# Kernel tuning notes

Hardware: AMD Instinct MI355X
Metric: run time of the kernel (lower is better)

The kernel has to match this reference:

```python
import jax, jax.numpy as jnp
import numpy as np

B, N, E = 4, 2048, 512
H = 8
HD = E // H  # 64
SCALE = HD ** -0.5


def setup_inputs() -> dict:
    key = jax.random.key(0)
    k1, k2, k3 = jax.random.split(key, 3)
    x = jax.random.normal(k1, (B, N, E), dtype=jnp.float32)
    # xavier-uniform-like scaling for weights
    w_qkv = jax.random.normal(k2, (3 * E, E), dtype=jnp.float32) * (2.0 / (4 * E)) ** 0.5
    b_qkv = jnp.zeros((3 * E,), dtype=jnp.float32)
    w_out = jax.random.normal(k3, (E, E), dtype=jnp.float32) * (1.0 / E) ** 0.5
    b_out = jnp.zeros((E,), dtype=jnp.float32)
    return {"x": x, "w_qkv": w_qkv, "b_qkv": b_qkv, "w_out": w_out, "b_out": b_out}


def reference(x, w_qkv, b_qkv, w_out, b_out):
    b_sz, n_patches, _ = x.shape
    # qkv projection: [B,N,3E] -> [B,N,3,H,HD] -> [B,H,3,N,HD]
    qkv = (jnp.einsum('bne,fe->bnf', x, w_qkv) + b_qkv)
    qkv = qkv.reshape(b_sz, n_patches, 3, H, HD).transpose(0, 3, 2, 1, 4)
    q, k, v = qkv[:, :, 0], qkv[:, :, 1], qkv[:, :, 2]  # each [B,H,N,HD]
    attn = jnp.einsum('bhqd,bhkd->bhqk', q * SCALE, k)  # [B,H,N,N]
    attn = jax.nn.softmax(attn, axis=-1)
    # attn_dropout p=0.0 -> identity in reference
    out = jnp.einsum('bhqk,bhkd->bhqd', attn, v)  # [B,H,N,HD]
    out = out.transpose(0, 2, 1, 3).reshape(b_sz, n_patches, E)
    out = jnp.einsum('bne,fe->bnf', out, w_out) + b_out
    return out
```

## Files before the change

kernel.cpp:

```cpp
#include <hip/hip_runtime.h>

#define BB   4
#define SEQ  2048
#define EMB  512
#define NH   8
#define HD   64

typedef __bf16 bf16x8 __attribute__((ext_vector_type(8)));
typedef float  f32x4  __attribute__((ext_vector_type(4)));

__device__ __forceinline__ short f2bf(float f) {
  union { float f; unsigned u; } v; v.f = f;
  unsigned r = v.u + 0x7fffu + ((v.u >> 16) & 1u);
  return (short)(r >> 16);
}

__device__ __forceinline__ void gl_lds16(const void* g, void* l) {
  __builtin_amdgcn_global_load_lds(
      (const __attribute__((address_space(1))) unsigned int*)g,
      (__attribute__((address_space(3))) unsigned int*)l, 16, 0, 0);
}

__global__ __launch_bounds__(256) void cast_f32_bf16(const float* __restrict__ in,
                                                     short* __restrict__ out, int n4) {
  int i = blockIdx.x * 256 + threadIdx.x;
  if (i < n4) {
    float4 v = ((const float4*)in)[i];
    short4 o;
    o.x = f2bf(v.x); o.y = f2bf(v.y); o.z = f2bf(v.z); o.w = f2bf(v.w);
    ((short4*)out)[i] = o;
  }
}

__global__ __launch_bounds__(256) void qkv_gemm(const short* __restrict__ A,
                                                const short* __restrict__ W,
                                                const float* __restrict__ bias,
                                                short* __restrict__ qo,
                                                short* __restrict__ ko,
                                                short* __restrict__ vto) {
  __shared__ __align__(16) short As[128 * 32];
  __shared__ __align__(16) short Bs[128 * 32];
  const int tid  = threadIdx.x;
  const int lane = tid & 63, wave = tid >> 6;
  const int wm = wave >> 1, wf = wave & 1;
  const int col = lane & 15, quad = lane >> 4;
  const int m0 = blockIdx.x * 128, f0 = blockIdx.y * 128;

  f32x4 acc[4][4];
#pragma unroll
  for (int i = 0; i < 4; ++i)
#pragma unroll
    for (int j = 0; j < 4; ++j)
#pragma unroll
      for (int r = 0; r < 4; ++r) acc[i][j][r] = 0.f;

  for (int kt = 0; kt < 512; kt += 32) {
    __syncthreads();
#pragma unroll
    for (int rd = 0; rd < 2; ++rd) {
      int slot = rd * 256 + tid;
      int r = slot >> 2, c8 = (slot & 3) * 8;
      gl_lds16(A + (size_t)(m0 + r) * 512 + kt + c8, (char*)As + rd * 4096 + wave * 1024);
      gl_lds16(W + (size_t)(f0 + r) * 512 + kt + c8, (char*)Bs + rd * 4096 + wave * 1024);
    }
    __syncthreads();
    bf16x8 af[4], bw[4];
#pragma unroll
    for (int i = 0; i < 4; ++i)
      af[i] = *(const bf16x8*)&As[(wm * 64 + i * 16 + col) * 32 + quad * 8];
#pragma unroll
    for (int j = 0; j < 4; ++j)
      bw[j] = *(const bf16x8*)&Bs[(wf * 64 + j * 16 + col) * 32 + quad * 8];
#pragma unroll
    for (int i = 0; i < 4; ++i)
#pragma unroll
      for (int j = 0; j < 4; ++j)
        acc[i][j] = __builtin_amdgcn_mfma_f32_16x16x32_bf16(af[i], bw[j], acc[i][j], 0, 0, 0);
  }

#pragma unroll
  for (int j = 0; j < 4; ++j) {
    const int f = f0 + wf * 64 + j * 16 + col;
    const float bv = bias[f];
    const int sIdx = f >> 9;
    const int h = (f >> 6) & 7;
    const int d = f & 63;
#pragma unroll
    for (int i = 0; i < 4; ++i) {
      const int mbase = m0 + wm * 64 + i * 16 + quad * 4;
      const int b = mbase >> 11;
      const int n = mbase & 2047;
      const size_t bh = (size_t)(b * NH + h);
      if (sIdx == 2) {
        short4 pk;
        pk.x = f2bf(acc[i][j][0] + bv);
        pk.y = f2bf(acc[i][j][1] + bv);
        pk.z = f2bf(acc[i][j][2] + bv);
        pk.w = f2bf(acc[i][j][3] + bv);
        *(short4*)&vto[(bh * HD + d) * SEQ + n] = pk;
      } else {
        short* __restrict__ dst = (sIdx == 0) ? qo : ko;
#pragma unroll
        for (int r = 0; r < 4; ++r)
          dst[(bh * SEQ + n + r) * HD + d] = f2bf(acc[i][j][r] + bv);
      }
    }
  }
}

__global__ __launch_bounds__(256) void attn_kernel(const short* __restrict__ q,
                                                   const short* __restrict__ k,
                                                   const short* __restrict__ vt,
                                                   short* __restrict__ o) {
  __shared__ __align__(16) short Ks[64 * 64];
  __shared__ __align__(16) short Vs[64 * 64];
  __shared__ __align__(16) short Ps[4 * 32 * 72];
  __shared__ float Ls[4 * 32];
  const int tid  = threadIdx.x;
  const int lane = tid & 63, wave = tid >> 6;
  const int col = lane & 15, quad = lane >> 4;
  const int bh = blockIdx.x & 31;
  const int q0 = (blockIdx.x >> 5) * 128;
  const size_t bhBase = (size_t)bh * SEQ * HD;

  bf16x8 qf[2][2];
#pragma unroll
  for (int t = 0; t < 2; ++t)
#pragma unroll
    for (int ks = 0; ks < 2; ++ks)
      qf[t][ks] = *(const bf16x8*)&q[bhBase +
          (size_t)(q0 + wave * 32 + t * 16 + col) * HD + ks * 32 + quad * 8];

  f32x4 oacc[2][4];
#pragma unroll
  for (int t = 0; t < 2; ++t)
#pragma unroll
    for (int nt = 0; nt < 4; ++nt)
#pragma unroll
      for (int r = 0; r < 4; ++r) oacc[t][nt][r] = 0.f;
  float lpart[2] = {0.f, 0.f};

  const int wbase = wave * 32 * 72;

  for (int n0 = 0; n0 < SEQ; n0 += 64) {
    __syncthreads();
#pragma unroll
    for (int c = 0; c < 4; ++c) {
      int slot = (c & 1) * 256 + wave * 64 + lane;
      int row = slot >> 3;
      int cb = (slot & 7) ^ (row & 7);
      if (c < 2)
        gl_lds16(k + bhBase + (size_t)(n0 + row) * HD + cb * 8,
                 (char*)Ks + (c & 1) * 4096 + wave * 1024);
      else
        gl_lds16(vt + bhBase + (size_t)row * SEQ + n0 + cb * 8,
                 (char*)Vs + (c & 1) * 4096 + wave * 1024);
    }
    __syncthreads();

    f32x4 sacc[4][2];
#pragma unroll
    for (int kt = 0; kt < 4; ++kt)
#pragma unroll
      for (int t = 0; t < 2; ++t)
#pragma unroll
        for (int r = 0; r < 4; ++r) sacc[kt][t][r] = 0.f;
#pragma unroll
    for (int kt = 0; kt < 4; ++kt)
#pragma unroll
      for (int ks = 0; ks < 2; ++ks) {
        bf16x8 kf = *(const bf16x8*)&Ks[(kt * 16 + col) * 64 +
                                        (((ks * 4 + quad) ^ (col & 7)) * 8)];
#pragma unroll
        for (int t = 0; t < 2; ++t)
          sacc[kt][t] = __builtin_amdgcn_mfma_f32_16x16x32_bf16(kf, qf[t][ks], sacc[kt][t], 0, 0, 0);
      }

#pragma unroll
    for (int kt = 0; kt < 4; ++kt)
#pragma unroll
      for (int t = 0; t < 2; ++t) {
        float p0 = __expf(0.125f * sacc[kt][t][0]);
        float p1 = __expf(0.125f * sacc[kt][t][1]);
        float p2 = __expf(0.125f * sacc[kt][t][2]);
        float p3 = __expf(0.125f * sacc[kt][t][3]);
        lpart[t] += (p0 + p1) + (p2 + p3);
        short4 pk; pk.x = f2bf(p0); pk.y = f2bf(p1); pk.z = f2bf(p2); pk.w = f2bf(p3);
        *(short4*)&Ps[wbase + (t * 16 + col) * 72 + kt * 16 + quad * 4] = pk;
      }

#pragma unroll
    for (int ks2 = 0; ks2 < 2; ++ks2) {
      bf16x8 pf[2];
#pragma unroll
      for (int t = 0; t < 2; ++t)
        pf[t] = *(const bf16x8*)&Ps[wbase + (t * 16 + col) * 72 + ks2 * 32 + quad * 8];
#pragma unroll
      for (int nt = 0; nt < 4; ++nt) {
        bf16x8 vf = *(const bf16x8*)&Vs[(nt * 16 + col) * 64 +
                                        (((ks2 * 4 + quad) ^ (col & 7)) * 8)];
#pragma unroll
        for (int t = 0; t < 2; ++t)
          oacc[t][nt] = __builtin_amdgcn_mfma_f32_16x16x32_bf16(pf[t], vf, oacc[t][nt], 0, 0, 0);
      }
    }
  }

#pragma unroll
  for (int t = 0; t < 2; ++t) {
    lpart[t] += __shfl_xor(lpart[t], 16);
    lpart[t] += __shfl_xor(lpart[t], 32);
    Ls[wave * 32 + t * 16 + col] = lpart[t];
  }

  const int b = bh >> 3, h = bh & 7;
#pragma unroll
  for (int t = 0; t < 2; ++t) {
    float rl[4];
#pragma unroll
    for (int r = 0; r < 4; ++r)
      rl[r] = 1.0f / Ls[wave * 32 + t * 16 + quad * 4 + r];
#pragma unroll
    for (int nt = 0; nt < 4; ++nt)
#pragma unroll
      for (int r = 0; r < 4; ++r) {
        const int n = q0 + wave * 32 + t * 16 + quad * 4 + r;
        o[((size_t)(b * SEQ + n)) * EMB + h * HD + nt * 16 + col] = f2bf(oacc[t][nt][r] * rl[r]);
      }
  }
}

__global__ __launch_bounds__(256) void proj_gemm(const short* __restrict__ A,
                                                 const short* __restrict__ W,
                                                 const float* __restrict__ bias,
                                                 float* __restrict__ out) {
  __shared__ __align__(16) short As[64 * 32];
  __shared__ __align__(16) short Bs[128 * 32];
  const int tid  = threadIdx.x;
  const int lane = tid & 63, wave = tid >> 6;
  const int wm = wave >> 1, wf = wave & 1;
  const int col = lane & 15, quad = lane >> 4;
  const int m0 = blockIdx.x * 64, f0 = blockIdx.y * 128;

  f32x4 acc[2][4];
#pragma unroll
  for (int i = 0; i < 2; ++i)
#pragma unroll
    for (int j = 0; j < 4; ++j)
#pragma unroll
      for (int r = 0; r < 4; ++r) acc[i][j][r] = 0.f;

  for (int kt = 0; kt < 512; kt += 32) {
    __syncthreads();
    gl_lds16(A + (size_t)(m0 + (tid >> 2)) * 512 + kt + (tid & 3) * 8,
             (char*)As + wave * 1024);
#pragma unroll
    for (int rd = 0; rd < 2; ++rd) {
      int slot = rd * 256 + tid;
      int r = slot >> 2, c8 = (slot & 3) * 8;
      gl_lds16(W + (size_t)(f0 + r) * 512 + kt + c8, (char*)Bs + rd * 4096 + wave * 1024);
    }
    __syncthreads();
    bf16x8 af[2], bw[4];
#pragma unroll
    for (int i = 0; i < 2; ++i)
      af[i] = *(const bf16x8*)&As[(wm * 32 + i * 16 + col) * 32 + quad * 8];
#pragma unroll
    for (int j = 0; j < 4; ++j)
      bw[j] = *(const bf16x8*)&Bs[(wf * 64 + j * 16 + col) * 32 + quad * 8];
#pragma unroll
    for (int i = 0; i < 2; ++i)
#pragma unroll
      for (int j = 0; j < 4; ++j)
        acc[i][j] = __builtin_amdgcn_mfma_f32_16x16x32_bf16(af[i], bw[j], acc[i][j], 0, 0, 0);
  }

#pragma unroll
  for (int j = 0; j < 4; ++j) {
    const int f = f0 + wf * 64 + j * 16 + col;
    const float bv = bias[f];
#pragma unroll
    for (int i = 0; i < 2; ++i) {
      const int mbase = m0 + wm * 32 + i * 16 + quad * 4;
#pragma unroll
      for (int r = 0; r < 4; ++r)
        out[(size_t)(mbase + r) * 512 + f] = acc[i][j][r] + bv;
    }
  }
}

extern "C" void kernel_launch(void* const* d_in, const int* in_sizes, int n_in,
                              void* d_out, int out_size, void* d_ws, size_t ws_size,
                              hipStream_t stream) {
  (void)in_sizes; (void)n_in; (void)out_size; (void)ws_size;
  const float* x     = (const float*)d_in[0];
  const float* w_qkv = (const float*)d_in[1];
  const float* b_qkv = (const float*)d_in[2];
  const float* w_out = (const float*)d_in[3];
  const float* b_out = (const float*)d_in[4];
  float* out = (float*)d_out;

  char* ws = (char*)d_ws;
  short* xb    = (short*)(ws + 0);
  short* wqkvb = (short*)(ws + 8388608);
  short* woutb = (short*)(ws + 9961472);
  short* qb    = (short*)(ws + 10485760);
  short* kb    = (short*)(ws + 18874368);
  short* vtb   = (short*)(ws + 27262976);
  short* ob    = (short*)(ws + 35651584);

  cast_f32_bf16<<<4096, 256, 0, stream>>>(x, xb, 1048576);
  cast_f32_bf16<<<768, 256, 0, stream>>>(w_qkv, wqkvb, 196608);
  cast_f32_bf16<<<256, 256, 0, stream>>>(w_out, woutb, 65536);
  qkv_gemm<<<dim3(64, 12), 256, 0, stream>>>(xb, wqkvb, b_qkv, qb, kb, vtb);
  attn_kernel<<<512, 256, 0, stream>>>(qb, kb, vtb, ob);
  proj_gemm<<<dim3(128, 4), 256, 0, stream>>>(ob, woutb, b_out, out);
}
```

Before: 180.1 us.

## Fuse cast kernels, widen GEMM K-tiles, fold softmax scale into Q with exp2

The three fp32-to-bf16 cast launches become one kernel that uses packed bf16 conversion. Both GEMMs move from a K tile of 32 to 64 with a swizzled LDS layout, halving the number of barrier pairs per K loop. The attention scale times log2(e) is folded into Q at the QKV epilogue, so softmax can use hardware exp2 with no per-element multiply. Attention load and LDS offsets are also precomputed outside the loop. Together these add LDS usage and register pressure, and Q is now stored pre-scaled in bf16, which changes rounding slightly.

After: 169.9 us. 1.06x faster.

```diff
diff --git a/kernel.cpp b/kernel.cpp
--- a/kernel.cpp
+++ b/kernel.cpp
@@ -5,6 +5,7 @@
 #define EMB  512
 #define NH   8
 #define HD   64
+#define QSCALE 0.18033688011f
 
 typedef __bf16 bf16x8 __attribute__((ext_vector_type(8)));
 typedef float  f32x4  __attribute__((ext_vector_type(4)));
@@ -15,21 +16,45 @@
   return (short)(r >> 16);
 }
 
+__device__ __forceinline__ unsigned pk_bf16(float a, float b) {
+#if __has_builtin(__builtin_amdgcn_cvt_pk_bf16_f32)
+  typedef __bf16 bf16v2 __attribute__((ext_vector_type(2)));
+  union { bf16v2 v; unsigned u; } cv;
+  cv.v = __builtin_amdgcn_cvt_pk_bf16_f32(a, b);
+  return cv.u;
+#else
+  return (unsigned)(unsigned short)f2bf(a) | ((unsigned)(unsigned short)f2bf(b) << 16);
+#endif
+}
+
+__device__ __forceinline__ float fexp2(float x) {
+#if __has_builtin(__builtin_amdgcn_exp2f)
+  return __builtin_amdgcn_exp2f(x);
+#else
+  return exp2f(x);
+#endif
+}
+
 __device__ __forceinline__ void gl_lds16(const void* g, void* l) {
   __builtin_amdgcn_global_load_lds(
       (const __attribute__((address_space(1))) unsigned int*)g,
       (__attribute__((address_space(3))) unsigned int*)l, 16, 0, 0);
 }
 
-__global__ __launch_bounds__(256) void cast_f32_bf16(const float* __restrict__ in,
-                                                     short* __restrict__ out, int n4) {
+__global__ __launch_bounds__(256) void cast_all(const float* __restrict__ x,
+                                                const float* __restrict__ wq,
+                                                const float* __restrict__ wo,
+                                                short* __restrict__ xb,
+                                                short* __restrict__ wqb,
+                                                short* __restrict__ wob) {
   int i = blockIdx.x * 256 + threadIdx.x;
-  if (i < n4) {
-    float4 v = ((const float4*)in)[i];
-    short4 o;
-    o.x = f2bf(v.x); o.y = f2bf(v.y); o.z = f2bf(v.z); o.w = f2bf(v.w);
-    ((short4*)out)[i] = o;
-  }
+  const float* src; short* dst; int off;
+  if (i < 1048576)      { src = x;  dst = xb;  off = i; }
+  else if (i < 1245184) { src = wq; dst = wqb; off = i - 1048576; }
+  else                  { src = wo; dst = wob; off = i - 1245184; }
+  float4 v = ((const float4*)src)[off];
+  uint2 o; o.x = pk_bf16(v.x, v.y); o.y = pk_bf16(v.z, v.w);
+  *(uint2*)&dst[off * 4] = o;
 }
 
 __global__ __launch_bounds__(256) void qkv_gemm(const short* __restrict__ A,
@@ -38,14 +63,32 @@
                                                 short* __restrict__ qo,
                                                 short* __restrict__ ko,
                                                 short* __restrict__ vto) {
-  __shared__ __align__(16) short As[128 * 32];
-  __shared__ __align__(16) short Bs[128 * 32];
+  __shared__ __align__(16) short As[128 * 64];
+  __shared__ __align__(16) short Bs[128 * 64];
   const int tid  = threadIdx.x;
   const int lane = tid & 63, wave = tid >> 6;
   const int wm = wave >> 1, wf = wave & 1;
   const int col = lane & 15, quad = lane >> 4;
   const int m0 = blockIdx.x * 128, f0 = blockIdx.y * 128;
 
+  const short* aSrc[4]; const short* wSrc[4];
+#pragma unroll
+  for (int rd = 0; rd < 4; ++rd) {
+    int slot = rd * 256 + tid;
+    int row = slot >> 3;
+    int cb  = (slot & 7) ^ (row & 7);
+    aSrc[rd] = A + (size_t)(m0 + row) * 512 + cb * 8;
+    wSrc[rd] = W + (size_t)(f0 + row) * 512 + cb * 8;
+  }
+  int aOff[2][4], bOff[2][4];
+#pragma unroll
+  for (int kk = 0; kk < 2; ++kk)
+#pragma unroll
+    for (int i = 0; i < 4; ++i) {
+      aOff[kk][i] = (wm * 64 + i * 16 + col) * 64 + (((kk * 4 + quad) ^ (col & 7)) * 8);
+      bOff[kk][i] = (wf * 64 + i * 16 + col) * 64 + (((kk * 4 + quad) ^ (col & 7)) * 8);
+    }
+
   f32x4 acc[4][4];
 #pragma unroll
   for (int i = 0; i < 4; ++i)
@@ -54,28 +97,28 @@
 #pragma unroll
       for (int r = 0; r < 4; ++r) acc[i][j][r] = 0.f;
 
-  for (int kt = 0; kt < 512; kt += 32) {
-    __syncthreads();
-#pragma unroll
-    for (int rd = 0; rd < 2; ++rd) {
-      int slot = rd * 256 + tid;
-      int r = slot >> 2, c8 = (slot & 3) * 8;
-      gl_lds16(A + (size_t)(m0 + r) * 512 + kt + c8, (char*)As + rd * 4096 + wave * 1024);
-      gl_lds16(W + (size_t)(f0 + r) * 512 + kt + c8, (char*)Bs + rd * 4096 + wave * 1024);
-    }
-    __syncthreads();
-    bf16x8 af[4], bw[4];
-#pragma unroll
-    for (int i = 0; i < 4; ++i)
-      af[i] = *(const bf16x8*)&As[(wm * 64 + i * 16 + col) * 32 + quad * 8];
-#pragma unroll
-    for (int j = 0; j < 4; ++j)
-      bw[j] = *(const bf16x8*)&Bs[(wf * 64 + j * 16 + col) * 32 + quad * 8];
-#pragma unroll
-    for (int i = 0; i < 4; ++i)
-#pragma unroll
-      for (int j = 0; j < 4; ++j)
-        acc[i][j] = __builtin_amdgcn_mfma_f32_16x16x32_bf16(af[i], bw[j], acc[i][j], 0, 0, 0);
+  for (int kt = 0; kt < 8; ++kt) {
+    __syncthreads();
+#pragma unroll
+    for (int rd = 0; rd < 4; ++rd) {
+      gl_lds16(aSrc[rd], (char*)As + rd * 4096 + wave * 1024);
+      gl_lds16(wSrc[rd], (char*)Bs + rd * 4096 + wave * 1024);
+      aSrc[rd] += 64; wSrc[rd] += 64;
+    }
+    __syncthreads();
+#pragma unroll
+    for (int kk = 0; kk < 2; ++kk) {
+      bf16x8 af[4], bw[4];
+#pragma unroll
+      for (int i = 0; i < 4; ++i) af[i] = *(const bf16x8*)&As[aOff[kk][i]];
+#pragma unroll
+      for (int j = 0; j < 4; ++j) bw[j] = *(const bf16x8*)&Bs[bOff[kk][j]];
+#pragma unroll
+      for (int i = 0; i < 4; ++i)
+#pragma unroll
+        for (int j = 0; j < 4; ++j)
+          acc[i][j] = __builtin_amdgcn_mfma_f32_16x16x32_bf16(af[i], bw[j], acc[i][j], 0, 0, 0);
+    }
   }
 
 #pragma unroll
@@ -92,17 +135,18 @@
       const int n = mbase & 2047;
       const size_t bh = (size_t)(b * NH + h);
       if (sIdx == 2) {
-        short4 pk;
-        pk.x = f2bf(acc[i][j][0] + bv);
-        pk.y = f2bf(acc[i][j][1] + bv);
-        pk.z = f2bf(acc[i][j][2] + bv);
-        pk.w = f2bf(acc[i][j][3] + bv);
-        *(short4*)&vto[(bh * HD + d) * SEQ + n] = pk;
+        uint2 pk;
+        pk.x = pk_bf16(acc[i][j][0] + bv, acc[i][j][1] + bv);
+        pk.y = pk_bf16(acc[i][j][2] + bv, acc[i][j][3] + bv);
+        *(uint2*)&vto[(bh * HD + d) * SEQ + n] = pk;
+      } else if (sIdx == 0) {
+#pragma unroll
+        for (int r = 0; r < 4; ++r)
+          qo[(bh * SEQ + n + r) * HD + d] = f2bf((acc[i][j][r] + bv) * QSCALE);
       } else {
-        short* __restrict__ dst = (sIdx == 0) ? qo : ko;
 #pragma unroll
         for (int r = 0; r < 4; ++r)
-          dst[(bh * SEQ + n + r) * HD + d] = f2bf(acc[i][j][r] + bv);
+          ko[(bh * SEQ + n + r) * HD + d] = f2bf(acc[i][j][r] + bv);
       }
     }
   }
@@ -131,6 +175,40 @@
       qf[t][ks] = *(const bf16x8*)&q[bhBase +
           (size_t)(q0 + wave * 32 + t * 16 + col) * HD + ks * 32 + quad * 8];
 
+  const int rowL = tid >> 3,         cbL = (tid & 7) ^ (rowL & 7);
+  const int rowH = (256 + tid) >> 3, cbH = (tid & 7) ^ (rowH & 7);
+  const short* ksrcL = k  + bhBase + (size_t)rowL * HD + cbL * 8;
+  const short* ksrcH = k  + bhBase + (size_t)rowH * HD + cbH * 8;
+  const short* vsrcL = vt + bhBase + (size_t)rowL * SEQ + cbL * 8;
+  const short* vsrcH = vt + bhBase + (size_t)rowH * SEQ + cbH * 8;
+  char* ldsKL = (char*)Ks + wave * 1024;
+  char* ldsKH = (char*)Ks + 4096 + wave * 1024;
+  char* ldsVL = (char*)Vs + wave * 1024;
+  char* ldsVH = (char*)Vs + 4096 + wave * 1024;
+
+  const int wbase = wave * 32 * 72;
+  int kfO[4][2], vfO[2][4], pwO[4][2], prO[2][2];
+#pragma unroll
+  for (int kt = 0; kt < 4; ++kt)
+#pragma unroll
+    for (int ks = 0; ks < 2; ++ks)
+      kfO[kt][ks] = (kt * 16 + col) * 64 + (((ks * 4 + quad) ^ (col & 7)) * 8);
+#pragma unroll
+  for (int ks2 = 0; ks2 < 2; ++ks2)
+#pragma unroll
+    for (int nt = 0; nt < 4; ++nt)
+      vfO[ks2][nt] = (nt * 16 + col) * 64 + (((ks2 * 4 + quad) ^ (col & 7)) * 8);
+#pragma unroll
+  for (int kt = 0; kt < 4; ++kt)
+#pragma unroll
+    for (int t = 0; t < 2; ++t)
+      pwO[kt][t] = wbase + (t * 16 + col) * 72 + kt * 16 + quad * 4;
+#pragma unroll
+  for (int t = 0; t < 2; ++t)
+#pragma unroll
+    for (int ks2 = 0; ks2 < 2; ++ks2)
+      prO[t][ks2] = wbase + (t * 16 + col) * 72 + ks2 * 32 + quad * 8;
+
   f32x4 oacc[2][4];
 #pragma unroll
   for (int t = 0; t < 2; ++t)
@@ -140,22 +218,13 @@
       for (int r = 0; r < 4; ++r) oacc[t][nt][r] = 0.f;
   float lpart[2] = {0.f, 0.f};
 
-  const int wbase = wave * 32 * 72;
-
   for (int n0 = 0; n0 < SEQ; n0 += 64) {
     __syncthreads();
-#pragma unroll
-    for (int c = 0; c < 4; ++c) {
-      int slot = (c & 1) * 256 + wave * 64 + lane;
-      int row = slot >> 3;
-      int cb = (slot & 7) ^ (row & 7);
-      if (c < 2)
-        gl_lds16(k + bhBase + (size_t)(n0 + row) * HD + cb * 8,
-                 (char*)Ks + (c & 1) * 4096 + wave * 1024);
-      else
-        gl_lds16(vt + bhBase + (size_t)row * SEQ + n0 + cb * 8,
-                 (char*)Vs + (c & 1) * 4096 + wave * 1024);
-    }
+    gl_lds16(ksrcL, ldsKL);
+    gl_lds16(ksrcH, ldsKH);
+    gl_lds16(vsrcL, ldsVL);
+    gl_lds16(vsrcH, ldsVH);
+    ksrcL += 64 * HD; ksrcH += 64 * HD; vsrcL += 64; vsrcH += 64;
     __syncthreads();
 
     f32x4 sacc[4][2];
@@ -169,8 +238,7 @@
     for (int kt = 0; kt < 4; ++kt)
 #pragma unroll
       for (int ks = 0; ks < 2; ++ks) {
-        bf16x8 kf = *(const bf16x8*)&Ks[(kt * 16 + col) * 64 +
-                                        (((ks * 4 + quad) ^ (col & 7)) * 8)];
+        bf16x8 kf = *(const bf16x8*)&Ks[kfO[kt][ks]];
 #pragma unroll
         for (int t = 0; t < 2; ++t)
           sacc[kt][t] = __builtin_amdgcn_mfma_f32_16x16x32_bf16(kf, qf[t][ks], sacc[kt][t], 0, 0, 0);
@@ -180,25 +248,23 @@
     for (int kt = 0; kt < 4; ++kt)
 #pragma unroll
       for (int t = 0; t < 2; ++t) {
-        float p0 = __expf(0.125f * sacc[kt][t][0]);
-        float p1 = __expf(0.125f * sacc[kt][t][1]);
-        float p2 = __expf(0.125f * sacc[kt][t][2]);
-        float p3 = __expf(0.125f * sacc[kt][t][3]);
+        float p0 = fexp2(sacc[kt][t][0]);
+        float p1 = fexp2(sacc[kt][t][1]);
+        float p2 = fexp2(sacc[kt][t][2]);
+        float p3 = fexp2(sacc[kt][t][3]);
         lpart[t] += (p0 + p1) + (p2 + p3);
-        short4 pk; pk.x = f2bf(p0); pk.y = f2bf(p1); pk.z = f2bf(p2); pk.w = f2bf(p3);
-        *(short4*)&Ps[wbase + (t * 16 + col) * 72 + kt * 16 + quad * 4] = pk;
+        uint2 w; w.x = pk_bf16(p0, p1); w.y = pk_bf16(p2, p3);
+        *(uint2*)&Ps[pwO[kt][t]] = w;
       }
 
 #pragma unroll
     for (int ks2 = 0; ks2 < 2; ++ks2) {
       bf16x8 pf[2];
 #pragma unroll
-      for (int t = 0; t < 2; ++t)
-        pf[t] = *(const bf16x8*)&Ps[wbase + (t * 16 + col) * 72 + ks2 * 32 + quad * 8];
+      for (int t = 0; t < 2; ++t) pf[t] = *(const bf16x8*)&Ps[prO[t][ks2]];
 #pragma unroll
       for (int nt = 0; nt < 4; ++nt) {
-        bf16x8 vf = *(const bf16x8*)&Vs[(nt * 16 + col) * 64 +
-                                        (((ks2 * 4 + quad) ^ (col & 7)) * 8)];
+        bf16x8 vf = *(const bf16x8*)&Vs[vfO[ks2][nt]];
 #pragma unroll
         for (int t = 0; t < 2; ++t)
           oacc[t][nt] = __builtin_amdgcn_mfma_f32_16x16x32_bf16(pf[t], vf, oacc[t][nt], 0, 0, 0);
@@ -234,14 +300,40 @@
                                                  const short* __restrict__ W,
                                                  const float* __restrict__ bias,
                                                  float* __restrict__ out) {
-  __shared__ __align__(16) short As[64 * 32];
-  __shared__ __align__(16) short Bs[128 * 32];
+  __shared__ __align__(16) short As[64 * 64];
+  __shared__ __align__(16) short Bs[128 * 64];
   const int tid  = threadIdx.x;
   const int lane = tid & 63, wave = tid >> 6;
   const int wm = wave >> 1, wf = wave & 1;
   const int col = lane & 15, quad = lane >> 4;
   const int m0 = blockIdx.x * 64, f0 = blockIdx.y * 128;
 
+  const short* aSrc[2]; const short* wSrc[4];
+#pragma unroll
+  for (int rd = 0; rd < 2; ++rd) {
+    int slot = rd * 256 + tid;
+    int row = slot >> 3;
+    int cb  = (slot & 7) ^ (row & 7);
+    aSrc[rd] = A + (size_t)(m0 + row) * 512 + cb * 8;
+  }
+#pragma unroll
+  for (int rd = 0; rd < 4; ++rd) {
+    int slot = rd * 256 + tid;
+    int row = slot >> 3;
+    int cb  = (slot & 7) ^ (row & 7);
+    wSrc[rd] = W + (size_t)(f0 + row) * 512 + cb * 8;
+  }
+  int aOff[2][2], bOff[2][4];
+#pragma unroll
+  for (int kk = 0; kk < 2; ++kk) {
+#pragma unroll
+    for (int i = 0; i < 2; ++i)
+      aOff[kk][i] = (wm * 32 + i * 16 + col) * 64 + (((kk * 4 + quad) ^ (col & 7)) * 8);
+#pragma unroll
+    for (int j = 0; j < 4; ++j)
+      bOff[kk][j] = (wf * 64 + j * 16 + col) * 64 + (((kk * 4 + quad) ^ (col & 7)) * 8);
+  }
+
   f32x4 acc[2][4];
 #pragma unroll
   for (int i = 0; i < 2; ++i)
@@ -250,29 +342,32 @@
 #pragma unroll
       for (int r = 0; r < 4; ++r) acc[i][j][r] = 0.f;
 
-  for (int kt = 0; kt < 512; kt += 32) {
-    __syncthreads();
-    gl_lds16(A + (size_t)(m0 + (tid >> 2)) * 512 + kt + (tid & 3) * 8,
-             (char*)As + wave * 1024);
+  for (int kt = 0; kt < 8; ++kt) {
+    __syncthreads();
 #pragma unroll
     for (int rd = 0; rd < 2; ++rd) {
-      int slot = rd * 256 + tid;
-      int r = slot >> 2, c8 = (slot & 3) * 8;
-      gl_lds16(W + (size_t)(f0 + r) * 512 + kt + c8, (char*)Bs + rd * 4096 + wave * 1024);
-    }
-    __syncthreads();
-    bf16x8 af[2], bw[4];
-#pragma unroll
-    for (int i = 0; i < 2; ++i)
-      af[i] = *(const bf16x8*)&As[(wm * 32 + i * 16 + col) * 32 + quad * 8];
-#pragma unroll
-    for (int j = 0; j < 4; ++j)
-      bw[j] = *(const bf16x8*)&Bs[(wf * 64 + j * 16 + col) * 32 + quad * 8];
-#pragma unroll
-    for (int i = 0; i < 2; ++i)
-#pragma unroll
-      for (int j = 0; j < 4; ++j)
-        acc[i][j] = __builtin_amdgcn_mfma_f32_16x16x32_bf16(af[i], bw[j], acc[i][j], 0, 0, 0);
+      gl_lds16(aSrc[rd], (char*)As + rd * 4096 + wave * 1024);
+      aSrc[rd] += 64;
+    }
+#pragma unroll
+    for (int rd = 0; rd < 4; ++rd) {
+      gl_lds16(wSrc[rd], (char*)Bs + rd * 4096 + wave * 1024);
+      wSrc[rd] += 64;
+    }
+    __syncthreads();
+#pragma unroll
+    for (int kk = 0; kk < 2; ++kk) {
+      bf16x8 af[2], bw[4];
+#pragma unroll
+      for (int i = 0; i < 2; ++i) af[i] = *(const bf16x8*)&As[aOff[kk][i]];
+#pragma unroll
+      for (int j = 0; j < 4; ++j) bw[j] = *(const bf16x8*)&Bs[bOff[kk][j]];
+#pragma unroll
+      for (int i = 0; i < 2; ++i)
+#pragma unroll
+        for (int j = 0; j < 4; ++j)
+          acc[i][j] = __builtin_amdgcn_mfma_f32_16x16x32_bf16(af[i], bw[j], acc[i][j], 0, 0, 0);
+    }
   }
 
 #pragma unroll
@@ -309,9 +404,7 @@
   short* vtb   = (short*)(ws + 27262976);
   short* ob    = (short*)(ws + 35651584);
 
-  cast_f32_bf16<<<4096, 256, 0, stream>>>(x, xb, 1048576);
-  cast_f32_bf16<<<768, 256, 0, stream>>>(w_qkv, wqkvb, 196608);
-  cast_f32_bf16<<<256, 256, 0, stream>>>(w_out, woutb, 65536);
+  cast_all<<<5120, 256, 0, stream>>>(x, w_qkv, w_out, xb, wqkvb, woutb);
   qkv_gemm<<<dim3(64, 12), 256, 0, stream>>>(xb, wqkvb, b_qkv, qb, kb, vtb);
   attn_kernel<<<512, 256, 0, stream>>>(qb, kb, vtb, ob);
   proj_gemm<<<dim3(128, 4), 256, 0, stream>>>(ob, woutb, b_out, out);
```
